# Kernel tuning notes

Hardware: AMD Instinct MI355X
Metric: run time of the kernel (lower is better)

The kernel has to match this reference:

```python
import math
import jax, jax.numpy as jnp
import numpy as np

V, D, A, H, FF, L, MD = 500, 512, 512, 8, 2048, 6, 512
HD = A // H
B, S, T = 32, 512, 128


def setup_inputs() -> dict:
    key = jax.random.key(0)
    ks = jax.random.split(key, 40)
    init = lambda k, shape: (jax.random.normal(k, shape, jnp.float32) * 0.02)
    inp = {
        'memory': jax.random.normal(ks[0], (B, S, MD), jnp.float32),
        'memory_lens': jax.random.randint(ks[1], (B,), S // 2, S + 1),
        'ys_in_pad': jax.random.randint(ks[2], (B, T), 0, V),
        'ys_in_lens': jax.random.randint(ks[3], (B,), T // 2, T + 1),
        'emb': init(ks[4], (V, D)),
        'w_out': init(ks[5], (D, V)),
        'b_out': jnp.zeros((V,), jnp.float32),
        # per-layer params stacked on leading L axis (consumed by lax.scan)
        'ln_sa_g': jnp.ones((L, D), jnp.float32), 'ln_sa_b': jnp.zeros((L, D), jnp.float32),
        'sa_wq': init(ks[6], (L, D, A)), 'sa_bq': init(ks[7], (L, A)),
        'sa_wk': init(ks[8], (L, D, A)), 'sa_bk': init(ks[9], (L, A)),
        'sa_wv': init(ks[10], (L, D, A)), 'sa_bv': init(ks[11], (L, A)),
        'sa_wo': init(ks[12], (L, A, D)), 'sa_bo': init(ks[13], (L, D)),
        'ln_ca_g': jnp.ones((L, D), jnp.float32), 'ln_ca_b': jnp.zeros((L, D), jnp.float32),
        'ca_wq': init(ks[14], (L, D, A)), 'ca_bq': init(ks[15], (L, A)),
        'ca_wk': init(ks[16], (L, MD, A)), 'ca_bk': init(ks[17], (L, A)),
        'ca_wv': init(ks[18], (L, MD, A)), 'ca_bv': init(ks[19], (L, A)),
        'ca_wo': init(ks[20], (L, A, D)), 'ca_bo': init(ks[21], (L, D)),
        'ln_ff_g': jnp.ones((L, D), jnp.float32), 'ln_ff_b': jnp.zeros((L, D), jnp.float32),
        'ff_w1': init(ks[22], (L, D, FF)), 'ff_b1': init(ks[23], (L, FF)),
        'ff_w2': init(ks[24], (L, FF, D)), 'ff_b2': init(ks[25], (L, D)),
    }
    return inp


def _layernorm(x, g, b, eps=1e-5):
    m = jnp.mean(x, axis=-1, keepdims=True)
    v = jnp.mean(jnp.square(x - m), axis=-1, keepdims=True)
    return (x - m) * jax.lax.rsqrt(v + eps) * g + b


def _mha(q_in, k_in, v_in, mask, wq, bq, wk, bk, wv, bv, wo, bo):
    # mask: True = disallowed. (B, T, S) for self-attn, (B, 1, S) for cross-attn.
    b_, tq, _ = q_in.shape
    ts = k_in.shape[1]
    q = (q_in @ wq + bq).reshape(b_, tq, H, HD).transpose(0, 2, 1, 3)
    k = (k_in @ wk + bk).reshape(b_, ts, H, HD).transpose(0, 2, 1, 3)
    v = (v_in @ wv + bv).reshape(b_, ts, H, HD).transpose(0, 2, 1, 3)
    s = jnp.einsum('bhtd,bhsd->bhts', q, k) / math.sqrt(HD)
    # penalize_abs_values_gt(limit=50, penalty=1e-4) is identity in the forward
    # pass (it only injects an auxiliary gradient during training).
    s = jnp.where(mask[:, None, :, :], -jnp.inf, s)
    a = jax.nn.softmax(s, axis=-1)  # dropout p=0.0 in this config
    o = jnp.einsum('bhts,bhsd->bhtd', a, v).transpose(0, 2, 1, 3).reshape(b_, tq, A)
    return o @ wo + bo


def _forward(memory, memory_lens, ys_in_pad, ys_in_lens, emb, w_out, b_out, layer_params):
    t = ys_in_pad.shape[1]
    # make_pad_mask | ~subsequent_mask  -> (B, T, T), True = masked
    pad = jnp.arange(t)[None, :] >= ys_in_lens[:, None]            # (B, T)
    causal = ~jnp.tril(jnp.ones((t, t), bool))                     # (T, T)
    tgt_mask = pad[:, None, :] | causal[None]                      # (B, T, T)
    mem_mask = (jnp.arange(memory.shape[1])[None, :] >= memory_lens[:, None])[:, None, :]

    # embedding + sinusoidal positional encoding (dropout in eval = identity)
    pos = jnp.arange(t, dtype=jnp.float32)[:, None]
    div = jnp.exp(jnp.arange(0, D, 2, dtype=jnp.float32) * (-math.log(10000.0) / D))
    pe = jnp.zeros((t, D), jnp.float32)
    pe = pe.at[:, 0::2].set(jnp.sin(pos * div)).at[:, 1::2].set(jnp.cos(pos * div))
    x = emb[ys_in_pad] * math.sqrt(D) + pe[None]

    def step(tgt, p):
        tn = _layernorm(tgt, p['ln_sa_g'], p['ln_sa_b'])
        tgt = tgt + _mha(tn, tn, tn, tgt_mask,
                         p['sa_wq'], p['sa_bq'], p['sa_wk'], p['sa_bk'],
                         p['sa_wv'], p['sa_bv'], p['sa_wo'], p['sa_bo'])
        tn = _layernorm(tgt, p['ln_ca_g'], p['ln_ca_b'])
        tgt = tgt + _mha(tn, memory, memory, mem_mask,
                         p['ca_wq'], p['ca_bq'], p['ca_wk'], p['ca_bk'],
                         p['ca_wv'], p['ca_bv'], p['ca_wo'], p['ca_bo'])
        tn = _layernorm(tgt, p['ln_ff_g'], p['ln_ff_b'])
        h = tn @ p['ff_w1'] + p['ff_b1']
        h = h * jax.nn.sigmoid(h)  # Swish
        tgt = tgt + h @ p['ff_w2'] + p['ff_b2']
        return tgt, None

    x, _ = jax.lax.scan(step, x, layer_params)
    return x @ w_out + b_out  # (B, T, V) logits


_LAYER_KEYS = ['ln_sa_g', 'ln_sa_b', 'sa_wq', 'sa_bq', 'sa_wk', 'sa_bk', 'sa_wv', 'sa_bv',
               'sa_wo', 'sa_bo', 'ln_ca_g', 'ln_ca_b', 'ca_wq', 'ca_bq', 'ca_wk', 'ca_bk',
               'ca_wv', 'ca_bv', 'ca_wo', 'ca_bo', 'ln_ff_g', 'ln_ff_b',
               'ff_w1', 'ff_b1', 'ff_w2', 'ff_b2']


def reference(memory, memory_lens, ys_in_pad, ys_in_lens, emb, w_out, b_out,
              ln_sa_g, ln_sa_b, sa_wq, sa_bq, sa_wk, sa_bk, sa_wv, sa_bv, sa_wo, sa_bo,
              ln_ca_g, ln_ca_b, ca_wq, ca_bq, ca_wk, ca_bk, ca_wv, ca_bv, ca_wo, ca_bo,
              ln_ff_g, ln_ff_b, ff_w1, ff_b1, ff_w2, ff_b2):
    loc = locals()
    layer_params = {k: loc[k] for k in _LAYER_KEYS}
    return _forward(memory, memory_lens, ys_in_pad, ys_in_lens, emb, w_out, b_out, layer_params)
```

## Files before the change

### kernel.cpp

```cpp
#include <hip/hip_runtime.h>
#include <hip/hip_bf16.h>
#include <hip/hip_fp16.h>

constexpr int Bc = 32, Sc = 512, Tc = 128, Dc = 512, Ac = 512, Hc = 8;
constexpr int HDc = 64, FFc = 2048, Lc = 6, Vc = 500;
constexpr int NTOK = Bc * Tc;
constexpr int NMEM = Bc * Sc;

typedef unsigned short u16;
typedef __attribute__((ext_vector_type(8))) short short8;
typedef __attribute__((ext_vector_type(4))) float f32x4;

__device__ __forceinline__ u16 bfc(float x) {
  __hip_bfloat16 h = __float2bfloat16(x);
  return *reinterpret_cast<u16*>(&h);
}

__device__ __forceinline__ void gload16(const void* g, void* l) {
  __builtin_amdgcn_global_load_lds(
      (const __attribute__((address_space(1))) unsigned int*)g,
      (__attribute__((address_space(3))) unsigned int*)l, 16, 0, 0);
}

template <int N>
__device__ __forceinline__ void waitv() {
  if constexpr (N == 8)      asm volatile("s_waitcnt vmcnt(8)" ::: "memory");
  else if constexpr (N == 6) asm volatile("s_waitcnt vmcnt(6)" ::: "memory");
  else if constexpr (N == 4) asm volatile("s_waitcnt vmcnt(4)" ::: "memory");
  else if constexpr (N == 3) asm volatile("s_waitcnt vmcnt(3)" ::: "memory");
  else                       asm volatile("s_waitcnt vmcnt(0)" ::: "memory");
  __builtin_amdgcn_sched_barrier(0);
}
__device__ __forceinline__ void barrier_fenced() {
  __builtin_amdgcn_s_barrier();
  __builtin_amdgcn_sched_barrier(0);
}
__device__ __forceinline__ void lgk0_barrier() {
  asm volatile("s_waitcnt lgkmcnt(0)" ::: "memory");
  __builtin_amdgcn_sched_barrier(0);
  __builtin_amdgcn_s_barrier();
  __builtin_amdgcn_sched_barrier(0);
}

__device__ __forceinline__ float wave_sum(float v) {
#pragma unroll
  for (int o = 32; o > 0; o >>= 1) v += __shfl_down(v, o);
  return v;
}

__global__ __launch_bounds__(256) void embed_pe_k(const int* __restrict__ ys,
                                                  const float* __restrict__ emb,
                                                  float* __restrict__ x) {
  int tok = blockIdx.x;
  int t = tok & (Tc - 1);
  int id = ys[tok];
  int j = threadIdx.x;
  int d0 = 2 * j;
  const float cdiv = -9.210340371976184f / (float)Dc;
  float div = expf((float)d0 * cdiv);
  float ang = (float)t * div;
  float pe0 = sinf(ang), pe1 = cosf(ang);
  const float sc = 22.627416997969522f;
  long base = (long)tok * Dc + d0;
  long ebase = (long)id * Dc + d0;
  x[base]     = emb[ebase]     * sc + pe0;
  x[base + 1] = emb[ebase + 1] * sc + pe1;
}

__global__ __launch_bounds__(256) void layernorm_k(const float* __restrict__ x,
                                                   const float* __restrict__ g,
                                                   const float* __restrict__ bta,
                                                   u16* __restrict__ out) {
  int row = blockIdx.x;
  int tid = threadIdx.x;
  const float* xr = x + (long)row * Dc;
  float2 xv = *(const float2*)(xr + tid * 2);
  float s  = xv.x + xv.y;
  float s2 = xv.x * xv.x + xv.y * xv.y;
  __shared__ float red[4], red2[4];
#pragma unroll
  for (int o = 32; o > 0; o >>= 1) {
    s  += __shfl_down(s, o);
    s2 += __shfl_down(s2, o);
  }
  if ((tid & 63) == 0) { red[tid >> 6] = s; red2[tid >> 6] = s2; }
  __syncthreads();
  float mean = (red[0] + red[1] + red[2] + red[3]) * (1.0f / Dc);
  float ms   = (red2[0] + red2[1] + red2[2] + red2[3]) * (1.0f / Dc);
  float var  = ms - mean * mean;
  float rstd = rsqrtf(var + 1e-5f);
  float dx0 = xv.x - mean, dx1 = xv.y - mean;
  ushort2 o;
  o.x = bfc(dx0 * rstd * g[2 * tid] + bta[2 * tid]);
  o.y = bfc(dx1 * rstd * g[2 * tid + 1] + bta[2 * tid + 1]);
  *(ushort2*)(out + (long)row * Dc + tid * 2) = o;
}

__global__ __launch_bounds__(256) void wtrans_k(const float* __restrict__ src,
                                                u16* __restrict__ dst,
                                                int K, int N, long srcStride, long dstStride) {
  int z = blockIdx.z;
  src += z * srcStride;
  dst += z * dstStride;
  __shared__ float t[32][33];
  int n0 = blockIdx.x * 32, k0 = blockIdx.y * 32;
  int tx = threadIdx.x & 31, ty = threadIdx.x >> 5;
#pragma unroll
  for (int i = 0; i < 4; i++) {
    int n = n0 + tx;
    t[ty + 8 * i][tx] = (n < N) ? src[(long)(k0 + ty + 8 * i) * N + n] : 0.0f;
  }
  __syncthreads();
#pragma unroll
  for (int i = 0; i < 4; i++) {
    dst[(long)(n0 + ty + 8 * i) * K + k0 + tx] = bfc(t[tx][ty + 8 * i]);
  }
}

struct PtrPack8 { const float* p[8]; };
__global__ __launch_bounds__(256) void wtrans8_k(PtrPack8 P, u16* __restrict__ Wt,
                                                 long PLW) {
  int z = blockIdx.z;
  int widx = z / 6, l = z - widx * 6;
  const float* src = P.p[widx] + (long)l * 262144;
  u16* dst = Wt + (long)widx * 262144 + (long)l * PLW;
  __shared__ float t[32][33];
  int n0 = blockIdx.x * 32, k0 = blockIdx.y * 32;
  int tx = threadIdx.x & 31, ty = threadIdx.x >> 5;
#pragma unroll
  for (int i = 0; i < 4; i++)
    t[ty + 8 * i][tx] = src[(long)(k0 + ty + 8 * i) * 512 + n0 + tx];
  __syncthreads();
#pragma unroll
  for (int i = 0; i < 4; i++)
    dst[(long)(n0 + ty + 8 * i) * 512 + k0 + tx] = bfc(t[tx][ty + 8 * i]);
}

__global__ __launch_bounds__(256) void f2b_k(const float* __restrict__ in,
                                             u16* __restrict__ out, long n) {
  long i = ((long)blockIdx.x * 256 + threadIdx.x) * 4;
  if (i >= n) return;
  float4 v = *(const float4*)(in + i);
  ushort4 o;
  o.x = bfc(v.x); o.y = bfc(v.y); o.z = bfc(v.z); o.w = bfc(v.w);
  *(ushort4*)(out + i) = o;
}

template <int BMW, int OMODE, bool BIAS, bool RES, bool SWISH, bool NCH, bool MLEN, bool MERGE>
__global__ __launch_bounds__(256) void mgemm_k(
    const u16* __restrict__ A, const u16* __restrict__ Bt,
    const float* __restrict__ bias0, const float* __restrict__ bias1,
    const float* __restrict__ bias2,
    void* __restrict__ Cv, const float* __restrict__ R, const int* __restrict__ mlens,
    const u16* __restrict__ A2, void* __restrict__ Cv2, int Mq,
    int N, int K, int lda, int ldb, int ldc, int nbi,
    long batAo, long batAi, long batBo, long batBi, long batCo, long batCi) {
  constexpr int BM = BMW * 32;
  constexpr int LPS = (BM == 128 ? 2 : 1) + 2;

  int gx = gridDim.x, gy = gridDim.y;
  int nwg = gx * gy * gridDim.z;
  int orig = blockIdx.x + gx * (blockIdx.y + gy * blockIdx.z);
  int q = nwg >> 3, r = nwg & 7, xcd = orig & 7, off = orig >> 3;
  int wgid = (xcd < r ? xcd * (q + 1) : r * (q + 1) + (xcd - r) * q) + off;
  int bxi = wgid % gx; int tmp = wgid / gx;
  int byi = tmp % gy;  int bzi = tmp / gy;

  int z = bzi;
  int bo = z / nbi, bi = z - bo * nbi;
  int m0 = byi * BM, n0 = bxi * 128;

  const u16* Ab;
  long coff;
  void* Cbase;
  if constexpr (MERGE) {
    if (bi == 0) {
      if (m0 >= Mq) return;
      Ab = A;
      coff = 0; Cbase = Cv;
    } else {
      if (MLEN && (m0 & 511) >= mlens[m0 >> 9]) return;
      Ab = A2;
      coff = (long)(bi - 1) * batCi; Cbase = Cv2;
    }
  } else {
    if constexpr (MLEN) {
      if ((m0 & 511) >= mlens[m0 >> 9]) return;
    }
    Ab = A + bo * batAo + bi * batAi;
    coff = bo * batCo + bi * batCi;
    Cbase = Cv;
  }
  const u16* Bb = Bt + bo * batBo + bi * batBi;
  const float* bias = nullptr;
  if constexpr (BIAS) bias = (bi == 0) ? bias0 : ((bi == 1) ? bias1 : bias2);

  __shared__ __align__(16) u16 As[3][BM * 32];
  __shared__ __align__(16) u16 Bs[3][128 * 32];

  int tid = threadIdx.x;
  int lane = tid & 63, wid = tid >> 6;
  int wm = wid >> 1, wn = wid & 1;
  int fr = lane & 15, grp = lane >> 4;

  f32x4 acc[BMW][4];
#pragma unroll
  for (int i = 0; i < BMW; i++)
#pragma unroll
    for (int j = 0; j < 4; j++) acc[i][j] = (f32x4){0.f, 0.f, 0.f, 0.f};

  const u16* ga = Ab + (long)(m0 + (tid >> 2)) * lda + ((tid & 3) << 3);
  const u16* gb = Bb + (long)(n0 + (tid >> 2)) * ldb + ((tid & 3) << 3);

  auto STAGE = [&](int buf, int kt) {
    u16* lA = &As[buf][tid * 8];
    u16* lB = &Bs[buf][tid * 8];
    gload16(ga + kt, lA);
    if constexpr (BM == 128) gload16(ga + kt + (long)64 * lda, lA + 2048);
    gload16(gb + kt, lB);
    gload16(gb + kt + (long)64 * ldb, lB + 2048);
  };

  auto COMPUTE = [&](int buf) {
    short8 av[BMW], bv[4];
#pragma unroll
    for (int i = 0; i < BMW; i++)
      av[i] = *(const short8*)&As[buf][(wm * BMW * 16 + i * 16 + fr) * 32 + grp * 8];
#pragma unroll
    for (int j = 0; j < 4; j++)
      bv[j] = *(const short8*)&Bs[buf][(wn * 64 + j * 16 + fr) * 32 + grp * 8];
#pragma unroll
    for (int i = 0; i < BMW; i++)
#pragma unroll
      for (int j = 0; j < 4; j++)
        acc[i][j] = __builtin_amdgcn_mfma_f32_16x16x32_bf16(av[i], bv[j], acc[i][j], 0, 0, 0);
  };

  int NT = K >> 5;
  STAGE(0, 0);
  STAGE(1, 32);
  int cbuf = 0, sbuf = 2, kt = 64;
  for (int t = 0; t < NT - 2; ++t) {
    STAGE(sbuf, kt); kt += 32;
    waitv<2 * LPS>();
    barrier_fenced();
    COMPUTE(cbuf);
    lgk0_barrier();
    sbuf = cbuf; cbuf = (cbuf == 2) ? 0 : cbuf + 1;
  }
  waitv<LPS>();  barrier_fenced(); COMPUTE(cbuf); lgk0_barrier();
  cbuf = (cbuf == 2) ? 0 : cbuf + 1;
  waitv<0>();    barrier_fenced(); COMPUTE(cbuf);

  int rbase = m0 + wm * BMW * 16 + grp * 4;
  int cbase = n0 + wn * 64 + fr;
#pragma unroll
  for (int i = 0; i < BMW; i++) {
#pragma unroll
    for (int j = 0; j < 4; j++) {
      int col = cbase + j * 16;
      if (NCH && col >= N) continue;
      float bb = 0.0f;
      if constexpr (BIAS) bb = bias[col];
#pragma unroll
      for (int r2 = 0; r2 < 4; r2++) {
        int row = rbase + i * 16 + r2;
        float v = acc[i][j][r2] + bb;
        long idx = coff + (long)row * ldc + col;
        if constexpr (RES) v += R[idx];
        if constexpr (SWISH) v = v / (1.0f + expf(-v));
        if constexpr (OMODE == 0) ((u16*)Cbase)[idx] = bfc(v);
        else ((float*)Cbase)[idx] = v;
      }
    }
  }
}

template <int SKV, int KVBLK, bool CAUSAL, int IQ>
__global__ __launch_bounds__(256) void fattn_k(
    const u16* __restrict__ Q, const u16* __restrict__ Kg, const u16* __restrict__ Vg,
    u16* __restrict__ O, const int* __restrict__ lens) {
  constexpr int NJ  = KVBLK / 16;
  constexpr int NKV = KVBLK / 32;
  constexpr int NT  = SKV / KVBLK;
  constexpr int KST = 72;
  constexpr int VST = KVBLK + 8;
  constexpr int WR  = 16 * IQ;
  constexpr int WGR = 64 * IQ;
  constexpr int CH  = KVBLK / 32;

  __shared__ __align__(16) u16 Ks[KVBLK * KST];
  __shared__ __align__(16) u16 Vs[64 * VST];
  __shared__ __align__(16) u16 Ps[WGR * VST];

  int bh = blockIdx.x; int b = bh >> 3, h = bh & 7;
  int row00 = blockIdx.y * WGR;
  int tid = threadIdx.x, lane = tid & 63, wid = tid >> 6;
  int fr = lane & 15, grp = lane >> 4;
  int len = lens[b];
  int row0w = row00 + wid * WR;

  short8 qa[IQ][2];
  {
    const u16* qp = Q + ((long)b * Tc + row0w + fr) * 512 + h * 64 + grp * 8;
#pragma unroll
    for (int i = 0; i < IQ; i++)
#pragma unroll
      for (int k2 = 0; k2 < 2; k2++)
        qa[i][k2] = *(const short8*)(qp + (long)i * 16 * 512 + k2 * 32);
  }

  float m_run[IQ][4], l_run[IQ][4];
  f32x4 acc_o[IQ][4];
#pragma unroll
  for (int i = 0; i < IQ; i++)
#pragma unroll
    for (int r = 0; r < 4; r++) { m_run[i][r] = -1e30f; l_run[i][r] = 0.0f; }
#pragma unroll
  for (int i = 0; i < IQ; i++)
#pragma unroll
    for (int j = 0; j < 4; j++) acc_o[i][j] = (f32x4){0.f, 0.f, 0.f, 0.f};

  const u16* Kbase = Kg + ((long)b * SKV) * 512 + h * 64;
  const u16* Vbase = Vg + ((long)b * SKV) * 512 + h * 64;

  int NTeff = NT;
  if constexpr (CAUSAL) NTeff = (row00 + WGR - 1) / KVBLK + 1;
  if (NTeff > NT) NTeff = NT;
  int lenT = (len + KVBLK - 1) / KVBLK;
  if (lenT < NTeff) NTeff = lenT;

  short8 kreg[CH], vreg[CH];
#pragma unroll
  for (int c = 0; c < CH; c++) {
    int idx = tid + 256 * c; int kv = idx >> 3, s = idx & 7;
    kreg[c] = *(const short8*)(Kbase + (long)kv * 512 + s * 8);
    vreg[c] = *(const short8*)(Vbase + (long)kv * 512 + s * 8);
  }

  for (int t = 0; t < NTeff; t++) {
    int kv0 = t * KVBLK;
    __syncthreads();
#pragma unroll
    for (int c = 0; c < CH; c++) {
      int idx = tid + 256 * c; int kv = idx >> 3, s = idx & 7;
      *(short8*)&Ks[kv * KST + s * 8] = kreg[c];
#pragma unroll
      for (int j = 0; j < 8; j++)
        Vs[(s * 8 + j) * VST + kv] = (u16)vreg[c][j];
    }
    __syncthreads();
    if (t + 1 < NTeff) {
      int kvn = kv0 + KVBLK;
#pragma unroll
      for (int c = 0; c < CH; c++) {
        int idx = tid + 256 * c; int kv = idx >> 3, s = idx & 7;
        kreg[c] = *(const short8*)(Kbase + (long)(kvn + kv) * 512 + s * 8);
        vreg[c] = *(const short8*)(Vbase + (long)(kvn + kv) * 512 + s * 8);
      }
    }

    int jmax = NJ, kvmax = NKV, jmaxW = NJ;
    if constexpr (CAUSAL) {
      jmax = (row0w + WR - 1 - kv0) / 16 + 1;
      if (jmax > NJ) jmax = NJ;
      kvmax = (row0w + WR - 1 - kv0) / 32 + 1;
      if (kvmax > NKV) kvmax = NKV;
      jmaxW = 2 * kvmax;
      if (jmaxW > NJ) jmaxW = NJ;
    }

    f32x4 accs[IQ][NJ];
    __builtin_amdgcn_s_setprio(1);
#pragma unroll
    for (int j = 0; j < NJ; j++) {
      if (CAUSAL && j >= jmax) continue;
      short8 bv0 = *(const short8*)&Ks[(j * 16 + fr) * KST + grp * 8];
      short8 bv1 = *(const short8*)&Ks[(j * 16 + fr) * KST + 32 + grp * 8];
#pragma unroll
      for (int i = 0; i < IQ; i++) {
        f32x4 a = __builtin_amdgcn_mfma_f32_16x16x32_bf16(qa[i][0], bv0, (f32x4){0.f,0.f,0.f,0.f}, 0, 0, 0);
        accs[i][j] = __builtin_amdgcn_mfma_f32_16x16x32_bf16(qa[i][1], bv1, a, 0, 0, 0);
      }
    }
    __builtin_amdgcn_s_setprio(0);

    float alpha[IQ][4];
#pragma unroll
    for (int i = 0; i < IQ; i++) {
#pragma unroll
      for (int r = 0; r < 4; r++) {
        int qrow = row0w + i * 16 + grp * 4 + r;
        float vmax = -1e30f;
#pragma unroll
        for (int j = 0; j < NJ; j++) {
          if (CAUSAL && j >= jmax) continue;
          int kvb = kv0 + j * 16 + fr;
          float s = accs[i][j][r] * 0.125f;
          bool msk = (kvb >= len) || (CAUSAL && kvb > qrow);
          s = msk ? -1e30f : s;
          accs[i][j][r] = s;
          vmax = fmaxf(vmax, s);
        }
        vmax = fmaxf(vmax, __shfl_xor(vmax, 1));
        vmax = fmaxf(vmax, __shfl_xor(vmax, 2));
        vmax = fmaxf(vmax, __shfl_xor(vmax, 4));
        vmax = fmaxf(vmax, __shfl_xor(vmax, 8));
        float mn = fmaxf(m_run[i][r], vmax);
        float al = __expf(m_run[i][r] - mn);
        m_run[i][r] = mn;
        alpha[i][r] = al;
        float rs = 0.0f;
#pragma unroll
        for (int j = 0; j < NJ; j++) {
          if (CAUSAL && j >= jmax) continue;
          float p = __expf(accs[i][j][r] - mn);
          accs[i][j][r] = p;
          rs += p;
        }
        rs += __shfl_xor(rs, 1);
        rs += __shfl_xor(rs, 2);
        rs += __shfl_xor(rs, 4);
        rs += __shfl_xor(rs, 8);
        l_run[i][r] = l_run[i][r] * al + rs;
      }
    }

#pragma unroll
    for (int i = 0; i < IQ; i++)
#pragma unroll
      for (int j = 0; j < NJ; j++) {
        if (CAUSAL && j >= jmaxW) continue;
#pragma unroll
        for (int r = 0; r < 4; r++) {
          int prow = wid * WR + i * 16 + grp * 4 + r;
          float pv = (CAUSAL && j >= jmax) ? 0.0f : accs[i][j][r];
          Ps[prow * VST + j * 16 + fr] = bfc(pv);
        }
      }

#pragma unroll
    for (int i = 0; i < IQ; i++)
#pragma unroll
      for (int jd = 0; jd < 4; jd++)
#pragma unroll
        for (int r = 0; r < 4; r++)
          acc_o[i][jd][r] *= alpha[i][r];

    __builtin_amdgcn_s_setprio(1);
#pragma unroll
    for (int kk = 0; kk < NKV; kk++) {
      if (CAUSAL && kk >= kvmax) continue;
      short8 pa[IQ];
#pragma unroll
      for (int i = 0; i < IQ; i++)
        pa[i] = *(const short8*)&Ps[(wid * WR + i * 16 + fr) * VST + kk * 32 + grp * 8];
#pragma unroll
      for (int jd = 0; jd < 4; jd++) {
        short8 vb = *(const short8*)&Vs[(jd * 16 + fr) * VST + kk * 32 + grp * 8];
#pragma unroll
        for (int i = 0; i < IQ; i++)
          acc_o[i][jd] = __builtin_amdgcn_mfma_f32_16x16x32_bf16(pa[i], vb, acc_o[i][jd], 0, 0, 0);
      }
    }
    __builtin_amdgcn_s_setprio(0);
  }

#pragma unroll
  for (int i = 0; i < IQ; i++) {
#pragma unroll
    for (int r = 0; r < 4; r++) {
      float inv = 1.0f / l_run[i][r];
      long tok = (long)b * Tc + row0w + i * 16 + grp * 4 + r;
#pragma unroll
      for (int jd = 0; jd < 4; jd++)
        O[tok * 512 + h * 64 + jd * 16 + fr] = bfc(acc_o[i][jd][r] * inv);
    }
  }
}

extern "C" void kernel_launch(void* const* d_in, const int* in_sizes, int n_in,
                              void* d_out, int out_size, void* d_ws, size_t ws_size,
                              hipStream_t stream) {
  const float* memory   = (const float*)d_in[0];
  const int*   mem_lens = (const int*)d_in[1];
  const int*   ys       = (const int*)d_in[2];
  const int*   ys_lens  = (const int*)d_in[3];
  const float* emb      = (const float*)d_in[4];
  const float* w_out    = (const float*)d_in[5];
  const float* b_out    = (const float*)d_in[6];
  const float* pp[26];
  for (int i = 0; i < 26; i++) pp[i] = (const float*)d_in[7 + i];

  constexpr long PLW = 4194304;
  constexpr long OFF_SAQ = 0, OFF_SAK = 262144, OFF_SAV = 524288, OFF_SAO = 786432,
                 OFF_CAQ = 1048576, OFF_CAK = 1310720, OFF_CAV = 1572864,
                 OFF_CAO = 1835008, OFF_FF1 = 2097152, OFF_FF2 = 3145728,
                 OFF_WOUT = 6 * PLW;
  u16*   Wt   = (u16*)d_ws;
  float* X    = (float*)(Wt + 25427968);
  u16*   TO   = (u16*)(X + 2097152);
  u16*   QKV  = TO + 2097152;
  u16*   memb = QKV + 3 * 2097152;
  u16*   Kb   = memb + 8388608;
  u16*   SCR  = Kb + 8388608;
  float* OUT  = (float*)d_out;

  PtrPack8 P8;
  P8.p[0] = pp[2];  P8.p[1] = pp[4];  P8.p[2] = pp[6];  P8.p[3] = pp[8];
  P8.p[4] = pp[12]; P8.p[5] = pp[14]; P8.p[6] = pp[16]; P8.p[7] = pp[18];
  wtrans8_k<<<dim3(16, 16, 48), 256, 0, stream>>>(P8, Wt, PLW);
  wtrans_k<<<dim3(64, 16, Lc), 256, 0, stream>>>(pp[22], Wt + OFF_FF1, 512, 2048, 1048576, PLW);
  wtrans_k<<<dim3(16, 64, Lc), 256, 0, stream>>>(pp[24], Wt + OFF_FF2, 2048, 512, 1048576, PLW);
  wtrans_k<<<dim3(16, 16, 1), 256, 0, stream>>>(w_out, Wt + OFF_WOUT, 512, 500, 0, 0);

  f2b_k<<<(NMEM * Dc / 4 + 255) / 256, 256, 0, stream>>>(memory, memb, (long)NMEM * Dc);
  embed_pe_k<<<NTOK, 256, 0, stream>>>(ys, emb, X);

  for (int l = 0; l < Lc; l++) {
    const u16* WtL = Wt + (long)l * PLW;

    layernorm_k<<<NTOK, 256, 0, stream>>>(X, pp[0] + (long)l * Dc, pp[1] + (long)l * Dc, TO);
    mgemm_k<4, 0, true, false, false, false, false, false><<<dim3(4, 32, 3), 256, 0, stream>>>(
        TO, WtL + OFF_SAQ, pp[3] + (long)l * Ac, pp[5] + (long)l * Ac, pp[7] + (long)l * Ac,
        QKV, nullptr, nullptr, nullptr, nullptr, 0,
        512, 512, 512, 512, 512, 3, 0, 0, 0, 262144, 0, 2097152);
    fattn_k<128, 128, true, 1><<<dim3(256, 2), 256, 0, stream>>>(
        QKV, QKV + 2097152, QKV + 2 * 2097152, TO, ys_lens);
    mgemm_k<2, 1, true, true, false, false, false, false><<<dim3(4, 64, 1), 256, 0, stream>>>(
        TO, WtL + OFF_SAO, pp[9] + (long)l * Dc, nullptr, nullptr, X, X, nullptr,
        nullptr, nullptr, 0,
        512, 512, 512, 512, 512, 1, 0, 0, 0, 0, 0, 0);

    layernorm_k<<<NTOK, 256, 0, stream>>>(X, pp[10] + (long)l * Dc, pp[11] + (long)l * Dc, TO);
    mgemm_k<4, 0, true, false, false, false, true, true><<<dim3(4, 128, 3), 256, 0, stream>>>(
        TO, WtL + OFF_CAQ, pp[13] + (long)l * Ac, pp[15] + (long)l * Ac, pp[17] + (long)l * Ac,
        QKV, nullptr, mem_lens, memb, Kb, 4096,
        512, 512, 512, 512, 512, 3, 0, 0, 0, 262144, 0, 8388608);
    fattn_k<512, 128, false, 1><<<dim3(256, 2), 256, 0, stream>>>(
        QKV, Kb, SCR, TO, mem_lens);
    mgemm_k<2, 1, true, true, false, false, false, false><<<dim3(4, 64, 1), 256, 0, stream>>>(
        TO, WtL + OFF_CAO, pp[19] + (long)l * Dc, nullptr, nullptr, X, X, nullptr,
        nullptr, nullptr, 0,
        512, 512, 512, 512, 512, 1, 0, 0, 0, 0, 0, 0);

    layernorm_k<<<NTOK, 256, 0, stream>>>(X, pp[20] + (long)l * Dc, pp[21] + (long)l * Dc, TO);
    mgemm_k<4, 0, true, false, true, false, false, false><<<dim3(16, 32, 1), 256, 0, stream>>>(
        TO, WtL + OFF_FF1, pp[23] + (long)l * FFc, nullptr, nullptr, SCR, nullptr, nullptr,
        nullptr, nullptr, 0,
        2048, 512, 512, 512, 2048, 1, 0, 0, 0, 0, 0, 0);
    mgemm_k<2, 1, true, true, false, false, false, false><<<dim3(4, 64, 1), 256, 0, stream>>>(
        SCR, WtL + OFF_FF2, pp[25] + (long)l * Dc, nullptr, nullptr, X, X, nullptr,
        nullptr, nullptr, 0,
        512, 2048, 2048, 2048, 512, 1, 0, 0, 0, 0, 0, 0);
  }

  f2b_k<<<(NTOK * Dc / 4 + 255) / 256, 256, 0, stream>>>(X, TO, (long)NTOK * Dc);
  mgemm_k<2, 1, true, false, false, true, false, false><<<dim3(4, 64, 1), 256, 0, stream>>>(
      TO, Wt + OFF_WOUT, b_out, nullptr, nullptr, OUT, nullptr, nullptr,
      nullptr, nullptr, 0,
      500, 512, 512, 512, 500, 1, 0, 0, 0, 0, 0, 0);
}
```

Measured before the change: 1.197 ms.

## Fold layernorm into following GEMMs via precomputed gamma-scaled weights and row stats

Removes the three per-layer layernorm kernels by folding gamma into the transposed weights and beta into a precomputed bias, then applying per-row mean/rstd correction in the consuming GEMM epilogue. The residual-producing GEMMs now also emit a bf16 copy of X and accumulate row sum and sum-of-squares via LDS and global atomics into per-stage stats buffers. This saves launches and a full read/write pass over the activations per layernorm. In exchange it adds atomics, extra epilogue stores and a bf16 input to the GEMM with unnormalised values, and it uses the E[x^2]-mean^2 variance form, which can lose precision.

```diff
diff --git a/kernel.cpp b/kernel.cpp
--- a/kernel.cpp
+++ b/kernel.cpp
@@ -42,15 +42,11 @@
   __builtin_amdgcn_sched_barrier(0);
 }
 
-__device__ __forceinline__ float wave_sum(float v) {
-#pragma unroll
-  for (int o = 32; o > 0; o >>= 1) v += __shfl_down(v, o);
-  return v;
-}
-
 __global__ __launch_bounds__(256) void embed_pe_k(const int* __restrict__ ys,
                                                   const float* __restrict__ emb,
-                                                  float* __restrict__ x) {
+                                                  float* __restrict__ x,
+                                                  u16* __restrict__ xb,
+                                                  float* __restrict__ st0) {
   int tok = blockIdx.x;
   int t = tok & (Tc - 1);
   int id = ys[tok];
@@ -63,42 +59,29 @@
   const float sc = 22.627416997969522f;
   long base = (long)tok * Dc + d0;
   long ebase = (long)id * Dc + d0;
-  x[base]     = emb[ebase]     * sc + pe0;
-  x[base + 1] = emb[ebase + 1] * sc + pe1;
-}
-
-__global__ __launch_bounds__(256) void layernorm_k(const float* __restrict__ x,
-                                                   const float* __restrict__ g,
-                                                   const float* __restrict__ bta,
-                                                   u16* __restrict__ out) {
-  int row = blockIdx.x;
-  int tid = threadIdx.x;
-  const float* xr = x + (long)row * Dc;
-  float2 xv = *(const float2*)(xr + tid * 2);
-  float s  = xv.x + xv.y;
-  float s2 = xv.x * xv.x + xv.y * xv.y;
+  float x0 = emb[ebase] * sc + pe0;
+  float x1 = emb[ebase + 1] * sc + pe1;
+  x[base] = x0; x[base + 1] = x1;
+  xb[base] = bfc(x0); xb[base + 1] = bfc(x1);
+  float s = x0 + x1, s2 = x0 * x0 + x1 * x1;
   __shared__ float red[4], red2[4];
 #pragma unroll
   for (int o = 32; o > 0; o >>= 1) {
     s  += __shfl_down(s, o);
     s2 += __shfl_down(s2, o);
   }
-  if ((tid & 63) == 0) { red[tid >> 6] = s; red2[tid >> 6] = s2; }
+  if ((j & 63) == 0) { red[j >> 6] = s; red2[j >> 6] = s2; }
   __syncthreads();
-  float mean = (red[0] + red[1] + red[2] + red[3]) * (1.0f / Dc);
-  float ms   = (red2[0] + red2[1] + red2[2] + red2[3]) * (1.0f / Dc);
-  float var  = ms - mean * mean;
-  float rstd = rsqrtf(var + 1e-5f);
-  float dx0 = xv.x - mean, dx1 = xv.y - mean;
-  ushort2 o;
-  o.x = bfc(dx0 * rstd * g[2 * tid] + bta[2 * tid]);
-  o.y = bfc(dx1 * rstd * g[2 * tid + 1] + bta[2 * tid + 1]);
-  *(ushort2*)(out + (long)row * Dc + tid * 2) = o;
+  if (j == 0) {
+    st0[(long)tok * 2]     = red[0] + red[1] + red[2] + red[3];
+    st0[(long)tok * 2 + 1] = red2[0] + red2[1] + red2[2] + red2[3];
+  }
 }
 
 __global__ __launch_bounds__(256) void wtrans_k(const float* __restrict__ src,
                                                 u16* __restrict__ dst,
-                                                int K, int N, long srcStride, long dstStride) {
+                                                int K, int N, long srcStride, long dstStride,
+                                                const float* __restrict__ gfold) {
   int z = blockIdx.z;
   src += z * srcStride;
   dst += z * dstStride;
@@ -108,7 +91,10 @@
 #pragma unroll
   for (int i = 0; i < 4; i++) {
     int n = n0 + tx;
-    t[ty + 8 * i][tx] = (n < N) ? src[(long)(k0 + ty + 8 * i) * N + n] : 0.0f;
+    int k = k0 + ty + 8 * i;
+    float v = (n < N) ? src[(long)k * N + n] : 0.0f;
+    if (gfold) v *= gfold[(long)z * 512 + k];
+    t[ty + 8 * i][tx] = v;
   }
   __syncthreads();
 #pragma unroll
@@ -117,23 +103,54 @@
   }
 }
 
-struct PtrPack8 { const float* p[8]; };
+struct PtrPack8 { const float* p[8]; const float* g[8]; };
 __global__ __launch_bounds__(256) void wtrans8_k(PtrPack8 P, u16* __restrict__ Wt,
                                                  long PLW) {
   int z = blockIdx.z;
   int widx = z / 6, l = z - widx * 6;
   const float* src = P.p[widx] + (long)l * 262144;
+  const float* gf = P.g[widx];
   u16* dst = Wt + (long)widx * 262144 + (long)l * PLW;
   __shared__ float t[32][33];
   int n0 = blockIdx.x * 32, k0 = blockIdx.y * 32;
   int tx = threadIdx.x & 31, ty = threadIdx.x >> 5;
 #pragma unroll
-  for (int i = 0; i < 4; i++)
-    t[ty + 8 * i][tx] = src[(long)(k0 + ty + 8 * i) * 512 + n0 + tx];
+  for (int i = 0; i < 4; i++) {
+    int k = k0 + ty + 8 * i;
+    float v = src[(long)k * 512 + n0 + tx];
+    if (gf) v *= gf[(long)l * 512 + k];
+    t[ty + 8 * i][tx] = v;
+  }
   __syncthreads();
 #pragma unroll
   for (int i = 0; i < 4; i++)
     dst[(long)(n0 + ty + 8 * i) * 512 + k0 + tx] = bfc(t[tx][ty + 8 * i]);
+}
+
+struct ColPack {
+  const float* W[5]; const float* g[5]; const float* b[5]; const float* bias[5];
+};
+__global__ __launch_bounds__(256) void colsum_k(ColPack P, float* __restrict__ cb,
+                                                float* __restrict__ db) {
+  int z = blockIdx.z;
+  int set = z / 6, l = z - set * 6;
+  const int Ns[5]   = {512, 512, 512, 512, 2048};
+  const long Ws[5]  = {262144, 262144, 262144, 262144, 1048576};
+  const int offs[5] = {0, 512, 1024, 1536, 2048};
+  int N = Ns[set];
+  int j = blockIdx.x * 256 + threadIdx.x;
+  if (j >= N) return;
+  const float* W = P.W[set] + (long)l * Ws[set];
+  const float* g = P.g[set] + (long)l * 512;
+  const float* b = P.b[set] + (long)l * 512;
+  float ca = 0.f, da = 0.f;
+  for (int k = 0; k < 512; k++) {
+    float w = W[(long)k * N + j];
+    ca += g[k] * w;
+    da += b[k] * w;
+  }
+  cb[(long)l * 4096 + offs[set] + j] = ca;
+  db[(long)l * 4096 + offs[set] + j] = da + P.bias[set][(long)l * N + j];
 }
 
 __global__ __launch_bounds__(256) void f2b_k(const float* __restrict__ in,
@@ -146,13 +163,18 @@
   *(ushort4*)(out + i) = o;
 }
 
-template <int BMW, int OMODE, bool BIAS, bool RES, bool SWISH, bool NCH, bool MLEN, bool MERGE>
+template <int BMW, int OMODE, bool BIAS, bool RES, bool SWISH, bool NCH, bool MLEN,
+          bool MERGE, int LNFM, bool SOUT>
 __global__ __launch_bounds__(256) void mgemm_k(
     const u16* __restrict__ A, const u16* __restrict__ Bt,
     const float* __restrict__ bias0, const float* __restrict__ bias1,
     const float* __restrict__ bias2,
     void* __restrict__ Cv, const float* __restrict__ R, const int* __restrict__ mlens,
     const u16* __restrict__ A2, void* __restrict__ Cv2, int Mq,
+    const float* __restrict__ cp0, const float* __restrict__ cp1,
+    const float* __restrict__ cp2,
+    const float* __restrict__ stats_in, float* __restrict__ stats_out,
+    u16* __restrict__ xb_out,
     int N, int K, int lda, int ldb, int ldc, int nbi,
     long batAo, long batAi, long batBo, long batBi, long batCo, long batCi) {
   constexpr int BM = BMW * 32;
@@ -197,6 +219,7 @@
 
   __shared__ __align__(16) u16 As[3][BM * 32];
   __shared__ __align__(16) u16 Bs[3][128 * 32];
+  __shared__ float statLDS[BM][2];
 
   int tid = threadIdx.x;
   int lane = tid & 63, wid = tid >> 6;
@@ -252,26 +275,78 @@
   cbuf = (cbuf == 2) ? 0 : cbuf + 1;
   waitv<0>();    barrier_fenced(); COMPUTE(cbuf);
 
+  bool dofold = (LNFM == 1) || (LNFM == 2 && bi == 0);
+  float psum[BMW * 4], psq[BMW * 4];
+  if constexpr (SOUT) {
+#pragma unroll
+    for (int t2 = 0; t2 < BMW * 4; t2++) { psum[t2] = 0.f; psq[t2] = 0.f; }
+  }
+
   int rbase = m0 + wm * BMW * 16 + grp * 4;
   int cbase = n0 + wn * 64 + fr;
 #pragma unroll
   for (int i = 0; i < BMW; i++) {
+    float mu_r[4], rs_r[4];
+    if constexpr (LNFM != 0) {
+      if (dofold) {
+#pragma unroll
+        for (int r2 = 0; r2 < 4; r2++) {
+          int row = rbase + i * 16 + r2;
+          float s = stats_in[(long)row * 2], s2 = stats_in[(long)row * 2 + 1];
+          float m = s * (1.0f / 512.0f);
+          float var = s2 * (1.0f / 512.0f) - m * m;
+          mu_r[r2] = m; rs_r[r2] = rsqrtf(var + 1e-5f);
+        }
+      }
+    }
 #pragma unroll
     for (int j = 0; j < 4; j++) {
       int col = cbase + j * 16;
       if (NCH && col >= N) continue;
-      float bb = 0.0f;
+      float bb = 0.0f, cc = 0.0f;
       if constexpr (BIAS) bb = bias[col];
+      if constexpr (LNFM != 0) {
+        if (dofold) {
+          const float* cp = (bi == 0) ? cp0 : ((bi == 1) ? cp1 : cp2);
+          cc = cp[col];
+        }
+      }
 #pragma unroll
       for (int r2 = 0; r2 < 4; r2++) {
         int row = rbase + i * 16 + r2;
-        float v = acc[i][j][r2] + bb;
+        float v = acc[i][j][r2];
+        if (LNFM != 0 && dofold) v = rs_r[r2] * (v - mu_r[r2] * cc) + bb;
+        else if constexpr (BIAS) v += bb;
         long idx = coff + (long)row * ldc + col;
         if constexpr (RES) v += R[idx];
         if constexpr (SWISH) v = v / (1.0f + expf(-v));
         if constexpr (OMODE == 0) ((u16*)Cbase)[idx] = bfc(v);
         else ((float*)Cbase)[idx] = v;
-      }
+        if constexpr (SOUT) {
+          xb_out[idx] = bfc(v);
+          psum[i * 4 + r2] += v;
+          psq[i * 4 + r2] += v * v;
+        }
+      }
+    }
+  }
+
+  if constexpr (SOUT) {
+    __syncthreads();
+    if (tid < BM) { statLDS[tid][0] = 0.f; statLDS[tid][1] = 0.f; }
+    __syncthreads();
+#pragma unroll
+    for (int i = 0; i < BMW; i++)
+#pragma unroll
+      for (int r2 = 0; r2 < 4; r2++) {
+        int rl = wm * BMW * 16 + grp * 4 + i * 16 + r2;
+        atomicAdd(&statLDS[rl][0], psum[i * 4 + r2]);
+        atomicAdd(&statLDS[rl][1], psq[i * 4 + r2]);
+      }
+    __syncthreads();
+    if (tid < BM) {
+      atomicAdd(&stats_out[(long)(m0 + tid) * 2],     statLDS[tid][0]);
+      atomicAdd(&stats_out[(long)(m0 + tid) * 2 + 1], statLDS[tid][1]);
     }
   }
 }
@@ -497,67 +572,91 @@
                  OFF_CAQ = 1048576, OFF_CAK = 1310720, OFF_CAV = 1572864,
                  OFF_CAO = 1835008, OFF_FF1 = 2097152, OFF_FF2 = 3145728,
                  OFF_WOUT = 6 * PLW;
-  u16*   Wt   = (u16*)d_ws;
-  float* X    = (float*)(Wt + 25427968);
-  u16*   TO   = (u16*)(X + 2097152);
-  u16*   QKV  = TO + 2097152;
-  u16*   memb = QKV + 3 * 2097152;
-  u16*   Kb   = memb + 8388608;
-  u16*   SCR  = Kb + 8388608;
-  float* OUT  = (float*)d_out;
+  u16*   Wt    = (u16*)d_ws;
+  float* X     = (float*)(Wt + 25427968);
+  u16*   TO    = (u16*)(X + 2097152);
+  u16*   QKV   = TO + 2097152;
+  u16*   memb  = QKV + 3 * 2097152;
+  u16*   Kb    = memb + 8388608;
+  u16*   SCR   = Kb + 8388608;
+  u16*   Xb    = SCR + 8388608;
+  float* stats = (float*)(Xb + 2097152);
+  float* c_buf = stats + 19 * 8192;
+  float* d_buf = c_buf + 6 * 4096;
+  float* OUT   = (float*)d_out;
+
+  hipMemsetAsync(stats, 0, 19 * 8192 * sizeof(float), stream);
 
   PtrPack8 P8;
   P8.p[0] = pp[2];  P8.p[1] = pp[4];  P8.p[2] = pp[6];  P8.p[3] = pp[8];
   P8.p[4] = pp[12]; P8.p[5] = pp[14]; P8.p[6] = pp[16]; P8.p[7] = pp[18];
+  P8.g[0] = pp[0];  P8.g[1] = pp[0];  P8.g[2] = pp[0];  P8.g[3] = nullptr;
+  P8.g[4] = pp[10]; P8.g[5] = nullptr; P8.g[6] = nullptr; P8.g[7] = nullptr;
   wtrans8_k<<<dim3(16, 16, 48), 256, 0, stream>>>(P8, Wt, PLW);
-  wtrans_k<<<dim3(64, 16, Lc), 256, 0, stream>>>(pp[22], Wt + OFF_FF1, 512, 2048, 1048576, PLW);
-  wtrans_k<<<dim3(16, 64, Lc), 256, 0, stream>>>(pp[24], Wt + OFF_FF2, 2048, 512, 1048576, PLW);
-  wtrans_k<<<dim3(16, 16, 1), 256, 0, stream>>>(w_out, Wt + OFF_WOUT, 512, 500, 0, 0);
+  wtrans_k<<<dim3(64, 16, Lc), 256, 0, stream>>>(pp[22], Wt + OFF_FF1, 512, 2048, 1048576, PLW, pp[20]);
+  wtrans_k<<<dim3(16, 64, Lc), 256, 0, stream>>>(pp[24], Wt + OFF_FF2, 2048, 512, 1048576, PLW, nullptr);
+  wtrans_k<<<dim3(16, 16, 1), 256, 0, stream>>>(w_out, Wt + OFF_WOUT, 512, 500, 0, 0, nullptr);
+
+  ColPack CP;
+  CP.W[0] = pp[2];  CP.W[1] = pp[4];  CP.W[2] = pp[6];  CP.W[3] = pp[12]; CP.W[4] = pp[22];
+  CP.g[0] = pp[0];  CP.g[1] = pp[0];  CP.g[2] = pp[0];  CP.g[3] = pp[10]; CP.g[4] = pp[20];
+  CP.b[0] = pp[1];  CP.b[1] = pp[1];  CP.b[2] = pp[1];  CP.b[3] = pp[11]; CP.b[4] = pp[21];
+  CP.bias[0] = pp[3]; CP.bias[1] = pp[5]; CP.bias[2] = pp[7]; CP.bias[3] = pp[13]; CP.bias[4] = pp[23];
+  colsum_k<<<dim3(8, 1, 30), 256, 0, stream>>>(CP, c_buf, d_buf);
 
   f2b_k<<<(NMEM * Dc / 4 + 255) / 256, 256, 0, stream>>>(memory, memb, (long)NMEM * Dc);
-  embed_pe_k<<<NTOK, 256, 0, stream>>>(ys, emb, X);
+  embed_pe_k<<<NTOK, 256, 0, stream>>>(ys, emb, X, Xb, stats);
 
   for (int l = 0; l < Lc; l++) {
     const u16* WtL = Wt + (long)l * PLW;
-
-    layernorm_k<<<NTOK, 256, 0, stream>>>(X, pp[0] + (long)l * Dc, pp[1] + (long)l * Dc, TO);
-    mgemm_k<4, 0, true, false, false, false, false, false><<<dim3(4, 32, 3), 256, 0, stream>>>(
-        TO, WtL + OFF_SAQ, pp[3] + (long)l * Ac, pp[5] + (long)l * Ac, pp[7] + (long)l * Ac,
+    const float* cL = c_buf + (long)l * 4096;
+    const float* dL = d_buf + (long)l * 4096;
+    float* stSA = stats + (long)(3 * l) * 8192;
+    float* stCA = stats + (long)(3 * l + 1) * 8192;
+    float* stFF = stats + (long)(3 * l + 2) * 8192;
+    float* stNX = stats + (long)(3 * l + 3) * 8192;
+
+    mgemm_k<4, 0, true, false, false, false, false, false, 1, false><<<dim3(4, 32, 3), 256, 0, stream>>>(
+        Xb, WtL + OFF_SAQ, dL + 0, dL + 512, dL + 1024,
         QKV, nullptr, nullptr, nullptr, nullptr, 0,
+        cL + 0, cL + 512, cL + 1024, stSA, nullptr, nullptr,
         512, 512, 512, 512, 512, 3, 0, 0, 0, 262144, 0, 2097152);
     fattn_k<128, 128, true, 1><<<dim3(256, 2), 256, 0, stream>>>(
         QKV, QKV + 2097152, QKV + 2 * 2097152, TO, ys_lens);
-    mgemm_k<2, 1, true, true, false, false, false, false><<<dim3(4, 64, 1), 256, 0, stream>>>(
+    mgemm_k<2, 1, true, true, false, false, false, false, 0, true><<<dim3(4, 64, 1), 256, 0, stream>>>(
         TO, WtL + OFF_SAO, pp[9] + (long)l * Dc, nullptr, nullptr, X, X, nullptr,
         nullptr, nullptr, 0,
+        nullptr, nullptr, nullptr, nullptr, stCA, Xb,
         512, 512, 512, 512, 512, 1, 0, 0, 0, 0, 0, 0);
 
-    layernorm_k<<<NTOK, 256, 0, stream>>>(X, pp[10] + (long)l * Dc, pp[11] + (long)l * Dc, TO);
-    mgemm_k<4, 0, true, false, false, false, true, true><<<dim3(4, 128, 3), 256, 0, stream>>>(
-        TO, WtL + OFF_CAQ, pp[13] + (long)l * Ac, pp[15] + (long)l * Ac, pp[17] + (long)l * Ac,
+    mgemm_k<4, 0, true, false, false, false, true, true, 2, false><<<dim3(4, 128, 3), 256, 0, stream>>>(
+        Xb, WtL + OFF_CAQ, dL + 1536, pp[15] + (long)l * Ac, pp[17] + (long)l * Ac,
         QKV, nullptr, mem_lens, memb, Kb, 4096,
+        cL + 1536, nullptr, nullptr, stCA, nullptr, nullptr,
         512, 512, 512, 512, 512, 3, 0, 0, 0, 262144, 0, 8388608);
     fattn_k<512, 128, false, 1><<<dim3(256, 2), 256, 0, stream>>>(
         QKV, Kb, SCR, TO, mem_lens);
-    mgemm_k<2, 1, true, true, false, false, false, false><<<dim3(4, 64, 1), 256, 0, stream>>>(
+    mgemm_k<2, 1, true, true, false, false, false, false, 0, true><<<dim3(4, 64, 1), 256, 0, stream>>>(
         TO, WtL + OFF_CAO, pp[19] + (long)l * Dc, nullptr, nullptr, X, X, nullptr,
         nullptr, nullptr, 0,
+        nullptr, nullptr, nullptr, nullptr, stFF, Xb,
         512, 512, 512, 512, 512, 1, 0, 0, 0, 0, 0, 0);
 
-    layernorm_k<<<NTOK, 256, 0, stream>>>(X, pp[20] + (long)l * Dc, pp[21] + (long)l * Dc, TO);
-    mgemm_k<4, 0, true, false, true, false, false, false><<<dim3(16, 32, 1), 256, 0, stream>>>(
-        TO, WtL + OFF_FF1, pp[23] + (long)l * FFc, nullptr, nullptr, SCR, nullptr, nullptr,
+    mgemm_k<4, 0, true, false, true, false, false, false, 1, false><<<dim3(16, 32, 1), 256, 0, stream>>>(
+        Xb, WtL + OFF_FF1, dL + 2048, nullptr, nullptr, SCR, nullptr, nullptr,
         nullptr, nullptr, 0,
+        cL + 2048, nullptr, nullptr, stFF, nullptr, nullptr,
         2048, 512, 512, 512, 2048, 1, 0, 0, 0, 0, 0, 0);
-    mgemm_k<2, 1, true, true, false, false, false, false><<<dim3(4, 64, 1), 256, 0, stream>>>(
+    mgemm_k<2, 1, true, true, false, false, false, false, 0, true><<<dim3(4, 64, 1), 256, 0, stream>>>(
         SCR, WtL + OFF_FF2, pp[25] + (long)l * Dc, nullptr, nullptr, X, X, nullptr,
         nullptr, nullptr, 0,
+        nullptr, nullptr, nullptr, nullptr, stNX, Xb,
         512, 2048, 2048, 2048, 512, 1, 0, 0, 0, 0, 0, 0);
   }
 
-  f2b_k<<<(NTOK * Dc / 4 + 255) / 256, 256, 0, stream>>>(X, TO, (long)NTOK * Dc);
-  mgemm_k<2, 1, true, false, false, true, false, false><<<dim3(4, 64, 1), 256, 0, stream>>>(
-      TO, Wt + OFF_WOUT, b_out, nullptr, nullptr, OUT, nullptr, nullptr,
+  mgemm_k<2, 1, true, false, false, true, false, false, 0, false><<<dim3(4, 64, 1), 256, 0, stream>>>(
+      Xb, Wt + OFF_WOUT, b_out, nullptr, nullptr, OUT, nullptr, nullptr,
       nullptr, nullptr, 0,
+      nullptr, nullptr, nullptr, nullptr, nullptr, nullptr,
       500, 512, 512, 512, 500, 1, 0, 0, 0, 0, 0, 0);
 }
```

Measured after the change: 1.324 ms. +10.5%, slower.
